# Optimization experiments

Measured on AMD Instinct MI355X. Metric: run time of the kernel, lower is better.

## Reference

```python
import jax, jax.numpy as jnp
import numpy as np

N = 50000


def gcn_conv(x, W, b, src, dst, deg_inv_sqrt):
    # h = x @ W, then symmetric-normalized aggregation with self-loops
    h = x @ W  # [N, out]
    norm = deg_inv_sqrt[src] * deg_inv_sqrt[dst]  # [E]
    agg = jax.ops.segment_sum(h[src] * norm[:, None], dst, num_segments=N)
    # self-loop contribution: norm_ii = deg_inv_sqrt[i]^2
    agg = agg + h * (deg_inv_sqrt * deg_inv_sqrt)[:, None]
    return agg + b


def setup_inputs() -> dict:
    key = jax.random.key(0)
    ks = jax.random.split(key, 8)
    F_in, H, C = 128, 128, 64
    x = jax.random.normal(ks[0], (N, F_in), dtype=jnp.float32)
    edge_index = jax.random.randint(ks[1], (2, 800000), 0, N, dtype=jnp.int64)
    s = 1.0 / np.sqrt(F_in)
    W1 = jax.random.uniform(ks[2], (F_in, H), jnp.float32, -s, s)
    b1 = jnp.zeros((H,), jnp.float32)
    W2 = jax.random.uniform(ks[3], (H, H), jnp.float32, -s, s)
    b2 = jnp.zeros((H,), jnp.float32)
    W3 = jax.random.uniform(ks[4], (H, C), jnp.float32, -s, s)
    b3 = jnp.zeros((C,), jnp.float32)
    return {"x": x, "edge_index": edge_index, "W1": W1, "b1": b1,
            "W2": W2, "b2": b2, "W3": W3, "b3": b3}


def reference(x, edge_index, W1, b1, W2, b2, W3, b3):
    src, dst = edge_index[0], edge_index[1]
    # degree with self-loops (edge weight 1): deg[i] = in-degree + 1
    deg = jnp.zeros((N,), x.dtype).at[dst].add(1.0) + 1.0
    dinv = jax.lax.rsqrt(deg)
    h = gcn_conv(x, W1, b1, src, dst, dinv)
    h = jax.nn.relu(h)  # dropout p=0 / eval -> identity
    h = gcn_conv(h, W2, b2, src, dst, dinv)
    h = jax.nn.relu(h)
    h = gcn_conv(h, W3, b3, src, dst, dinv)
    return jax.nn.log_softmax(h, axis=-1)
```

## Files before the change

kernel.cpp:

```cpp
#include <hip/hip_runtime.h>
#include <math.h>

typedef short short8 __attribute__((ext_vector_type(8)));
typedef float floatx4 __attribute__((ext_vector_type(4)));

__device__ __forceinline__ float4 ld4(const float* p) { return *reinterpret_cast<const float4*>(p); }
__device__ __forceinline__ void st4(float* p, float4 v) { *reinterpret_cast<float4*>(p) = v; }

__device__ __forceinline__ float bf2f(unsigned int u) { return __uint_as_float(u << 16); }
__device__ __forceinline__ unsigned int f2bf1(float f) {
    unsigned int x = __float_as_uint(f);
    return (x + 0x7fffu + ((x >> 16) & 1u)) >> 16;
}
__device__ __forceinline__ unsigned int f2bf2(float lo, float hi) {
    return f2bf1(lo) | (f2bf1(hi) << 16);
}
__device__ __forceinline__ void unpack8(uint4 v, float* f) {
    f[0] = bf2f(v.x & 0xffffu); f[1] = bf2f(v.x >> 16);
    f[2] = bf2f(v.y & 0xffffu); f[3] = bf2f(v.y >> 16);
    f[4] = bf2f(v.z & 0xffffu); f[5] = bf2f(v.z >> 16);
    f[6] = bf2f(v.w & 0xffffu); f[7] = bf2f(v.w >> 16);
}

__global__ __launch_bounds__(256) void k_count(const int* __restrict__ dst, int* __restrict__ deg,
                                               int* __restrict__ rank, int E) {
    int e = blockIdx.x * 256 + threadIdx.x;
    if (e < E) rank[e] = atomicAdd(&deg[dst[e]], 1);
}

__global__ __launch_bounds__(256) void k_reduce256(const int* __restrict__ deg, int* __restrict__ bsum, int n) {
    __shared__ int s[256];
    int t = threadIdx.x;
    int i = blockIdx.x * 256 + t;
    s[t] = (i < n) ? deg[i] : 0;
    __syncthreads();
    for (int off = 128; off > 0; off >>= 1) {
        if (t < off) s[t] += s[t + off];
        __syncthreads();
    }
    if (t == 0) bsum[blockIdx.x] = s[0];
}

__global__ __launch_bounds__(256) void k_scan_small(const int* __restrict__ bsum, int* __restrict__ boff, int nb) {
    __shared__ int s[256];
    int t = threadIdx.x;
    int v = (t < nb) ? bsum[t] : 0;
    s[t] = v;
    __syncthreads();
    for (int off = 1; off < 256; off <<= 1) {
        int x = (t >= off) ? s[t - off] : 0;
        __syncthreads();
        s[t] += x;
        __syncthreads();
    }
    if (t < nb) boff[t] = s[t] - v;
}

__global__ __launch_bounds__(256) void k_scan_final(const int* __restrict__ deg, const int* __restrict__ boff,
                                                    int* __restrict__ row_off, float* __restrict__ dinv, int n) {
    __shared__ int s[256];
    int t = threadIdx.x;
    int i = blockIdx.x * 256 + t;
    int v = (i < n) ? deg[i] : 0;
    s[t] = v;
    __syncthreads();
    for (int off = 1; off < 256; off <<= 1) {
        int x = (t >= off) ? s[t - off] : 0;
        __syncthreads();
        s[t] += x;
        __syncthreads();
    }
    int incl = s[t] + boff[blockIdx.x];
    if (i < n) {
        row_off[i] = incl - v;
        dinv[i]    = 1.0f / sqrtf((float)v + 1.0f);
        if (i == n - 1) row_off[n] = incl;
    }
}

__global__ __launch_bounds__(256) void k_fill(const int* __restrict__ src, const int* __restrict__ dst,
                                              const int* __restrict__ rank, const int* __restrict__ roff,
                                              const float* __restrict__ dinv, int2* __restrict__ cpair, int E) {
    int e = blockIdx.x * 256 + threadIdx.x;
    if (e < E) {
        int s = src[e], d = dst[e];
        int pos = roff[d] + rank[e];
        cpair[pos] = make_int2(s, __float_as_int(dinv[s] * dinv[d]));
    }
}

__global__ __launch_bounds__(256) void k_prepW(const float* __restrict__ W1, const float* __restrict__ W2,
                                               const float* __restrict__ W3, unsigned short* __restrict__ Wt1,
                                               unsigned short* __restrict__ Wt2, unsigned short* __restrict__ Wt3) {
    int t = blockIdx.x * 256 + threadIdx.x;
    if (t < 16384) {
        int k = t & 127, n = t >> 7;
        Wt1[n * 128 + k] = (unsigned short)f2bf1(W1[(size_t)k * 128 + n]);
    } else if (t < 32768) {
        int u = t - 16384;
        int k = u & 127, n = u >> 7;
        Wt2[n * 128 + k] = (unsigned short)f2bf1(W2[(size_t)k * 128 + n]);
    } else if (t < 40960) {
        int u = t - 32768;
        int k = u & 127, n = u >> 7;
        Wt3[n * 128 + k] = (unsigned short)f2bf1(W3[(size_t)k * 64 + n]);
    }
}

template <int NC, bool XF32>
__global__ __launch_bounds__(256) void k_gemm_mfma(const void* __restrict__ Xv, const unsigned short* __restrict__ Wt,
                                                   unsigned short* __restrict__ O, int nrows) {
    constexpr int LDR = 136;
    __shared__ unsigned short sX[64 * LDR];
    __shared__ unsigned short sB[NC * LDR];

    const int tid  = threadIdx.x;
    const int row0 = blockIdx.x * 64;

    if constexpr (XF32) {
        const float* X = (const float*)Xv;
#pragma unroll
        for (int i = 0; i < 4; ++i) {
            int idx = tid + i * 256;
            int r = idx >> 4, c8 = idx & 15;
            int grow = row0 + r;
            uint4 v = make_uint4(0, 0, 0, 0);
            if (grow < nrows) {
                float4 a = ld4(X + (size_t)grow * 128 + c8 * 8);
                float4 b = ld4(X + (size_t)grow * 128 + c8 * 8 + 4);
                v = make_uint4(f2bf2(a.x, a.y), f2bf2(a.z, a.w), f2bf2(b.x, b.y), f2bf2(b.z, b.w));
            }
            *reinterpret_cast<uint4*>(&sX[r * LDR + c8 * 8]) = v;
        }
    } else {
        const unsigned short* X = (const unsigned short*)Xv;
#pragma unroll
        for (int i = 0; i < 4; ++i) {
            int idx = tid + i * 256;
            int r = idx >> 4, c8 = idx & 15;
            int grow = row0 + r;
            uint4 v = make_uint4(0, 0, 0, 0);
            if (grow < nrows) v = *reinterpret_cast<const uint4*>(X + (size_t)grow * 128 + c8 * 8);
            *reinterpret_cast<uint4*>(&sX[r * LDR + c8 * 8]) = v;
        }
    }
#pragma unroll
    for (int i = 0; i < NC / 16; ++i) {
        int idx = tid + i * 256;
        int n = idx >> 4, c8 = idx & 15;
        *reinterpret_cast<uint4*>(&sB[n * LDR + c8 * 8]) =
            *reinterpret_cast<const uint4*>(Wt + (size_t)n * 128 + c8 * 8);
    }
    __syncthreads();

    const int lane = tid & 63;
    const int wave = tid >> 6;
    const int l15  = lane & 15;
    const int quad = lane >> 4;

    floatx4 acc[NC / 16];
#pragma unroll
    for (int j = 0; j < NC / 16; ++j) acc[j] = (floatx4){0.f, 0.f, 0.f, 0.f};

    const unsigned short* xbase = &sX[(wave * 16 + l15) * LDR + quad * 8];
#pragma unroll
    for (int kk = 0; kk < 4; ++kk) {
        short8 xb = *reinterpret_cast<const short8*>(xbase + kk * 32);
#pragma unroll
        for (int j = 0; j < NC / 16; ++j) {
            short8 wa = *reinterpret_cast<const short8*>(&sB[(j * 16 + l15) * LDR + quad * 8 + kk * 32]);
            acc[j] = __builtin_amdgcn_mfma_f32_16x16x32_bf16(wa, xb, acc[j], 0, 0, 0);
        }
    }

    int xrow = row0 + wave * 16 + l15;
    if (xrow < nrows) {
#pragma unroll
        for (int j = 0; j < NC / 16; ++j) {
            uint2 o = make_uint2(f2bf2(acc[j][0], acc[j][1]), f2bf2(acc[j][2], acc[j][3]));
            *reinterpret_cast<uint2*>(O + (size_t)xrow * NC + j * 16 + quad * 4) = o;
        }
    }
}

__global__ __launch_bounds__(256) void k_agg_relu(const unsigned short* __restrict__ H, const int* __restrict__ roff,
                                                  const int2* __restrict__ cpair, const float* __restrict__ dinv,
                                                  const float* __restrict__ bias, unsigned short* __restrict__ O, int n) {
    int t    = blockIdx.x * 256 + threadIdx.x;
    int node = t >> 4;
    int f8   = (t & 15) * 8;
    if (node >= n) return;

    float di = dinv[node];
    float sc = di * di;
    float a[8];
    {
        uint4 hv = *reinterpret_cast<const uint4*>(H + (size_t)node * 128 + f8);
        float h[8];
        unpack8(hv, h);
#pragma unroll
        for (int i = 0; i < 8; ++i) a[i] = h[i] * sc;
    }

    int e  = roff[node];
    int e1 = roff[node + 1];
    for (; e + 3 < e1; e += 4) {
        int2 p[4];
        uint4 v[4];
#pragma unroll
        for (int u = 0; u < 4; ++u) p[u] = cpair[e + u];
#pragma unroll
        for (int u = 0; u < 4; ++u) v[u] = *reinterpret_cast<const uint4*>(H + (size_t)p[u].x * 128 + f8);
#pragma unroll
        for (int u = 0; u < 4; ++u) {
            float nu = __int_as_float(p[u].y);
            float g[8];
            unpack8(v[u], g);
#pragma unroll
            for (int i = 0; i < 8; ++i) a[i] += g[i] * nu;
        }
    }
    for (; e < e1; ++e) {
        int2 p0 = cpair[e];
        float n0 = __int_as_float(p0.y);
        uint4 v0 = *reinterpret_cast<const uint4*>(H + (size_t)p0.x * 128 + f8);
        float g0[8];
        unpack8(v0, g0);
#pragma unroll
        for (int i = 0; i < 8; ++i) a[i] += g0[i] * n0;
    }

    float4 b0 = ld4(bias + f8);
    float4 b1 = ld4(bias + f8 + 4);
    float bb[8] = {b0.x, b0.y, b0.z, b0.w, b1.x, b1.y, b1.z, b1.w};
#pragma unroll
    for (int i = 0; i < 8; ++i) a[i] = fmaxf(a[i] + bb[i], 0.0f);

    uint4 ov = make_uint4(f2bf2(a[0], a[1]), f2bf2(a[2], a[3]), f2bf2(a[4], a[5]), f2bf2(a[6], a[7]));
    *reinterpret_cast<uint4*>(O + (size_t)node * 128 + f8) = ov;
}

__global__ __launch_bounds__(256) void k_agg_softmax(const unsigned short* __restrict__ H, const int* __restrict__ roff,
                                                     const int2* __restrict__ cpair, const float* __restrict__ dinv,
                                                     const float* __restrict__ bias, float* __restrict__ O, int n) {
    int t    = blockIdx.x * 256 + threadIdx.x;
    int node = t >> 3;
    int f8   = (t & 7) * 8;
    if (node >= n) return;

    float di = dinv[node];
    float sc = di * di;
    float a[8];
    {
        uint4 hv = *reinterpret_cast<const uint4*>(H + (size_t)node * 64 + f8);
        float h[8];
        unpack8(hv, h);
#pragma unroll
        for (int i = 0; i < 8; ++i) a[i] = h[i] * sc;
    }

    int e  = roff[node];
    int e1 = roff[node + 1];
    for (; e + 3 < e1; e += 4) {
        int2 p[4];
        uint4 v[4];
#pragma unroll
        for (int u = 0; u < 4; ++u) p[u] = cpair[e + u];
#pragma unroll
        for (int u = 0; u < 4; ++u) v[u] = *reinterpret_cast<const uint4*>(H + (size_t)p[u].x * 64 + f8);
#pragma unroll
        for (int u = 0; u < 4; ++u) {
            float nu = __int_as_float(p[u].y);
            float g[8];
            unpack8(v[u], g);
#pragma unroll
            for (int i = 0; i < 8; ++i) a[i] += g[i] * nu;
        }
    }
    for (; e < e1; ++e) {
        int2 p0 = cpair[e];
        float n0 = __int_as_float(p0.y);
        uint4 v0 = *reinterpret_cast<const uint4*>(H + (size_t)p0.x * 64 + f8);
        float g0[8];
        unpack8(v0, g0);
#pragma unroll
        for (int i = 0; i < 8; ++i) a[i] += g0[i] * n0;
    }

    float4 b0 = ld4(bias + f8);
    float4 b1 = ld4(bias + f8 + 4);
    float bb[8] = {b0.x, b0.y, b0.z, b0.w, b1.x, b1.y, b1.z, b1.w};
    float v[8];
#pragma unroll
    for (int i = 0; i < 8; ++i) v[i] = a[i] + bb[i];

    float m = v[0];
#pragma unroll
    for (int i = 1; i < 8; ++i) m = fmaxf(m, v[i]);
    m = fmaxf(m, __shfl_xor(m, 1));
    m = fmaxf(m, __shfl_xor(m, 2));
    m = fmaxf(m, __shfl_xor(m, 4));

    float ssum = 0.0f;
#pragma unroll
    for (int i = 0; i < 8; ++i) ssum += expf(v[i] - m);
    ssum += __shfl_xor(ssum, 1);
    ssum += __shfl_xor(ssum, 2);
    ssum += __shfl_xor(ssum, 4);
    float ls = logf(ssum);

    float* op = O + (size_t)node * 64 + f8;
    st4(op, make_float4(v[0] - m - ls, v[1] - m - ls, v[2] - m - ls, v[3] - m - ls));
    st4(op + 4, make_float4(v[4] - m - ls, v[5] - m - ls, v[6] - m - ls, v[7] - m - ls));
}

extern "C" void kernel_launch(void* const* d_in, const int* in_sizes, int n_in,
                              void* d_out, int out_size, void* d_ws, size_t ws_size,
                              hipStream_t stream) {
    const float* x  = (const float*)d_in[0];
    const int*   ei = (const int*)d_in[1];
    const float* W1 = (const float*)d_in[2];
    const float* b1 = (const float*)d_in[3];
    const float* W2 = (const float*)d_in[4];
    const float* b2 = (const float*)d_in[5];
    const float* W3 = (const float*)d_in[6];
    const float* b3 = (const float*)d_in[7];
    float* out = (float*)d_out;

    const int N = in_sizes[0] / 128;
    const int E = in_sizes[1] / 2;
    const int* src = ei;
    const int* dst = ei + E;

    char* ws = (char*)d_ws;
    size_t off = 0;
    auto alloc = [&](size_t bytes) -> char* {
        char* p = ws + off;
        off = (off + bytes + 255) & ~(size_t)255;
        return p;
    };
    int nb = (N + 255) / 256;
    int*   deg     = (int*)alloc((size_t)N * 4);
    int*   row_off = (int*)alloc(((size_t)N + 1) * 4);
    float* dinv    = (float*)alloc((size_t)N * 4);
    int*   bsum    = (int*)alloc((size_t)nb * 4);
    int*   boff    = (int*)alloc((size_t)nb * 4);
    int*   rank    = (int*)alloc((size_t)E * 4);
    int2*  cpair   = (int2*)alloc((size_t)E * 8);
    unsigned short* Wt1  = (unsigned short*)alloc(128 * 128 * 2);
    unsigned short* Wt2  = (unsigned short*)alloc(128 * 128 * 2);
    unsigned short* Wt3  = (unsigned short*)alloc(64 * 128 * 2);
    unsigned short* bufA = (unsigned short*)alloc((size_t)N * 128 * 2);
    unsigned short* bufB = (unsigned short*)alloc((size_t)N * 128 * 2);
    unsigned short* bufC = (unsigned short*)alloc((size_t)N * 64 * 2);
    (void)ws_size; (void)n_in; (void)out_size;

    hipMemsetAsync(deg, 0, (size_t)N * 4, stream);
    k_count<<<(E + 255) / 256, 256, 0, stream>>>(dst, deg, rank, E);
    k_reduce256<<<nb, 256, 0, stream>>>(deg, bsum, N);
    k_scan_small<<<1, 256, 0, stream>>>(bsum, boff, nb);
    k_scan_final<<<nb, 256, 0, stream>>>(deg, boff, row_off, dinv, N);
    k_fill<<<(E + 255) / 256, 256, 0, stream>>>(src, dst, rank, row_off, dinv, cpair, E);

    k_prepW<<<(40960 + 255) / 256, 256, 0, stream>>>(W1, W2, W3, Wt1, Wt2, Wt3);

    int gemm_blocks = (N + 63) / 64;
    k_gemm_mfma<128, true><<<gemm_blocks, 256, 0, stream>>>(x, Wt1, bufA, N);
    k_agg_relu<<<((size_t)N * 16 + 255) / 256, 256, 0, stream>>>(bufA, row_off, cpair, dinv, b1, bufB, N);
    k_gemm_mfma<128, false><<<gemm_blocks, 256, 0, stream>>>(bufB, Wt2, bufA, N);
    k_agg_relu<<<((size_t)N * 16 + 255) / 256, 256, 0, stream>>>(bufA, row_off, cpair, dinv, b2, bufB, N);
    k_gemm_mfma<64, false><<<gemm_blocks, 256, 0, stream>>>(bufB, Wt3, bufC, N);
    k_agg_softmax<<<((size_t)N * 8 + 255) / 256, 256, 0, stream>>>(bufC, row_off, cpair, dinv, b3, out, N);
}
```

Before: 257.7 us.

## Fuse aggregation+ReLU with the next layer's GEMM and unroll gathers by eight

```diff
diff --git a/kernel.cpp b/kernel.cpp
--- a/kernel.cpp
+++ b/kernel.cpp
@@ -107,45 +107,30 @@
     }
 }
 
-template <int NC, bool XF32>
-__global__ __launch_bounds__(256) void k_gemm_mfma(const void* __restrict__ Xv, const unsigned short* __restrict__ Wt,
-                                                   unsigned short* __restrict__ O, int nrows) {
+__global__ __launch_bounds__(256) void k_gemm1(const float* __restrict__ X, const unsigned short* __restrict__ Wt,
+                                               unsigned short* __restrict__ O, int nrows) {
     constexpr int LDR = 136;
     __shared__ unsigned short sX[64 * LDR];
-    __shared__ unsigned short sB[NC * LDR];
+    __shared__ unsigned short sB[128 * LDR];
 
     const int tid  = threadIdx.x;
     const int row0 = blockIdx.x * 64;
 
-    if constexpr (XF32) {
-        const float* X = (const float*)Xv;
-#pragma unroll
-        for (int i = 0; i < 4; ++i) {
-            int idx = tid + i * 256;
-            int r = idx >> 4, c8 = idx & 15;
-            int grow = row0 + r;
-            uint4 v = make_uint4(0, 0, 0, 0);
-            if (grow < nrows) {
-                float4 a = ld4(X + (size_t)grow * 128 + c8 * 8);
-                float4 b = ld4(X + (size_t)grow * 128 + c8 * 8 + 4);
-                v = make_uint4(f2bf2(a.x, a.y), f2bf2(a.z, a.w), f2bf2(b.x, b.y), f2bf2(b.z, b.w));
-            }
-            *reinterpret_cast<uint4*>(&sX[r * LDR + c8 * 8]) = v;
-        }
-    } else {
-        const unsigned short* X = (const unsigned short*)Xv;
-#pragma unroll
-        for (int i = 0; i < 4; ++i) {
-            int idx = tid + i * 256;
-            int r = idx >> 4, c8 = idx & 15;
-            int grow = row0 + r;
-            uint4 v = make_uint4(0, 0, 0, 0);
-            if (grow < nrows) v = *reinterpret_cast<const uint4*>(X + (size_t)grow * 128 + c8 * 8);
-            *reinterpret_cast<uint4*>(&sX[r * LDR + c8 * 8]) = v;
-        }
-    }
-#pragma unroll
-    for (int i = 0; i < NC / 16; ++i) {
+#pragma unroll
+    for (int i = 0; i < 4; ++i) {
+        int idx = tid + i * 256;
+        int r = idx >> 4, c8 = idx & 15;
+        int grow = row0 + r;
+        uint4 v = make_uint4(0, 0, 0, 0);
+        if (grow < nrows) {
+            float4 a = ld4(X + (size_t)grow * 128 + c8 * 8);
+            float4 b = ld4(X + (size_t)grow * 128 + c8 * 8 + 4);
+            v = make_uint4(f2bf2(a.x, a.y), f2bf2(a.z, a.w), f2bf2(b.x, b.y), f2bf2(b.z, b.w));
+        }
+        *reinterpret_cast<uint4*>(&sX[r * LDR + c8 * 8]) = v;
+    }
+#pragma unroll
+    for (int i = 0; i < 8; ++i) {
         int idx = tid + i * 256;
         int n = idx >> 4, c8 = idx & 15;
         *reinterpret_cast<uint4*>(&sB[n * LDR + c8 * 8]) =
@@ -158,16 +143,16 @@
     const int l15  = lane & 15;
     const int quad = lane >> 4;
 
-    floatx4 acc[NC / 16];
-#pragma unroll
-    for (int j = 0; j < NC / 16; ++j) acc[j] = (floatx4){0.f, 0.f, 0.f, 0.f};
+    floatx4 acc[8];
+#pragma unroll
+    for (int j = 0; j < 8; ++j) acc[j] = (floatx4){0.f, 0.f, 0.f, 0.f};
 
     const unsigned short* xbase = &sX[(wave * 16 + l15) * LDR + quad * 8];
 #pragma unroll
     for (int kk = 0; kk < 4; ++kk) {
         short8 xb = *reinterpret_cast<const short8*>(xbase + kk * 32);
 #pragma unroll
-        for (int j = 0; j < NC / 16; ++j) {
+        for (int j = 0; j < 8; ++j) {
             short8 wa = *reinterpret_cast<const short8*>(&sB[(j * 16 + l15) * LDR + quad * 8 + kk * 32]);
             acc[j] = __builtin_amdgcn_mfma_f32_16x16x32_bf16(wa, xb, acc[j], 0, 0, 0);
         }
@@ -175,69 +160,124 @@
 
     int xrow = row0 + wave * 16 + l15;
     if (xrow < nrows) {
+#pragma unroll
+        for (int j = 0; j < 8; ++j) {
+            uint2 o = make_uint2(f2bf2(acc[j][0], acc[j][1]), f2bf2(acc[j][2], acc[j][3]));
+            *reinterpret_cast<uint2*>(O + (size_t)xrow * 128 + j * 16 + quad * 4) = o;
+        }
+    }
+}
+
+template <int NC>
+__global__ __launch_bounds__(256) void k_agg_gemm(const unsigned short* __restrict__ H, const int* __restrict__ roff,
+                                                  const int2* __restrict__ cpair, const float* __restrict__ dinv,
+                                                  const float* __restrict__ bias, const unsigned short* __restrict__ Wt,
+                                                  unsigned short* __restrict__ O, int n) {
+    constexpr int LDR = 136;
+    __shared__ unsigned short sX[64 * LDR];
+
+    const int tid  = threadIdx.x;
+    const int row0 = blockIdx.x * 64;
+    const int g    = tid >> 4;
+    const int f8   = (tid & 15) * 8;
+
+    float4 b0 = ld4(bias + f8);
+    float4 b1 = ld4(bias + f8 + 4);
+    float bb[8] = {b0.x, b0.y, b0.z, b0.w, b1.x, b1.y, b1.z, b1.w};
+
+#pragma unroll
+    for (int p = 0; p < 4; ++p) {
+        int node = row0 + p * 16 + g;
+        float a[8] = {0.f, 0.f, 0.f, 0.f, 0.f, 0.f, 0.f, 0.f};
+        if (node < n) {
+            float di = dinv[node];
+            float sc = di * di;
+            uint4 hv = *reinterpret_cast<const uint4*>(H + (size_t)node * 128 + f8);
+            float h[8];
+            unpack8(hv, h);
+#pragma unroll
+            for (int i = 0; i < 8; ++i) a[i] = h[i] * sc;
+
+            int e  = roff[node];
+            int e1 = roff[node + 1];
+            for (; e + 7 < e1; e += 8) {
+                int2 pr[8];
+                uint4 v[8];
+#pragma unroll
+                for (int u = 0; u < 8; ++u) pr[u] = cpair[e + u];
+#pragma unroll
+                for (int u = 0; u < 8; ++u) v[u] = *reinterpret_cast<const uint4*>(H + (size_t)pr[u].x * 128 + f8);
+#pragma unroll
+                for (int u = 0; u < 8; ++u) {
+                    float nu = __int_as_float(pr[u].y);
+                    float gg[8];
+                    unpack8(v[u], gg);
+#pragma unroll
+                    for (int i = 0; i < 8; ++i) a[i] += gg[i] * nu;
+                }
+            }
+            if (e + 3 < e1) {
+                int2 pr[4];
+                uint4 v[4];
+#pragma unroll
+                for (int u = 0; u < 4; ++u) pr[u] = cpair[e + u];
+#pragma unroll
+                for (int u = 0; u < 4; ++u) v[u] = *reinterpret_cast<const uint4*>(H + (size_t)pr[u].x * 128 + f8);
+#pragma unroll
+                for (int u = 0; u < 4; ++u) {
+                    float nu = __int_as_float(pr[u].y);
+                    float gg[8];
+                    unpack8(v[u], gg);
+#pragma unroll
+                    for (int i = 0; i < 8; ++i) a[i] += gg[i] * nu;
+                }
+                e += 4;
+            }
+            for (; e < e1; ++e) {
+                int2 p0 = cpair[e];
+                float n0 = __int_as_float(p0.y);
+                uint4 v0 = *reinterpret_cast<const uint4*>(H + (size_t)p0.x * 128 + f8);
+                float g0[8];
+                unpack8(v0, g0);
+#pragma unroll
+                for (int i = 0; i < 8; ++i) a[i] += g0[i] * n0;
+            }
+#pragma unroll
+            for (int i = 0; i < 8; ++i) a[i] = fmaxf(a[i] + bb[i], 0.0f);
+        }
+        uint4 ov = make_uint4(f2bf2(a[0], a[1]), f2bf2(a[2], a[3]), f2bf2(a[4], a[5]), f2bf2(a[6], a[7]));
+        *reinterpret_cast<uint4*>(&sX[(p * 16 + g) * LDR + f8]) = ov;
+    }
+    __syncthreads();
+
+    const int lane = tid & 63;
+    const int wave = tid >> 6;
+    const int l15  = lane & 15;
+    const int quad = lane >> 4;
+
+    floatx4 acc[NC / 16];
+#pragma unroll
+    for (int j = 0; j < NC / 16; ++j) acc[j] = (floatx4){0.f, 0.f, 0.f, 0.f};
+
+    const unsigned short* xbase = &sX[(wave * 16 + l15) * LDR + quad * 8];
+#pragma unroll
+    for (int kk = 0; kk < 4; ++kk) {
+        short8 xb = *reinterpret_cast<const short8*>(xbase + kk * 32);
+#pragma unroll
+        for (int j = 0; j < NC / 16; ++j) {
+            short8 wa = *reinterpret_cast<const short8*>(Wt + (size_t)(j * 16 + l15) * 128 + quad * 8 + kk * 32);
+            acc[j] = __builtin_amdgcn_mfma_f32_16x16x32_bf16(wa, xb, acc[j], 0, 0, 0);
+        }
+    }
+
+    int xrow = row0 + wave * 16 + l15;
+    if (xrow < n) {
 #pragma unroll
         for (int j = 0; j < NC / 16; ++j) {
             uint2 o = make_uint2(f2bf2(acc[j][0], acc[j][1]), f2bf2(acc[j][2], acc[j][3]));
             *reinterpret_cast<uint2*>(O + (size_t)xrow * NC + j * 16 + quad * 4) = o;
         }
     }
-}
-
-__global__ __launch_bounds__(256) void k_agg_relu(const unsigned short* __restrict__ H, const int* __restrict__ roff,
-                                                  const int2* __restrict__ cpair, const float* __restrict__ dinv,
-                                                  const float* __restrict__ bias, unsigned short* __restrict__ O, int n) {
-    int t    = blockIdx.x * 256 + threadIdx.x;
-    int node = t >> 4;
-    int f8   = (t & 15) * 8;
-    if (node >= n) return;
-
-    float di = dinv[node];
-    float sc = di * di;
-    float a[8];
-    {
-        uint4 hv = *reinterpret_cast<const uint4*>(H + (size_t)node * 128 + f8);
-        float h[8];
-        unpack8(hv, h);
-#pragma unroll
-        for (int i = 0; i < 8; ++i) a[i] = h[i] * sc;
-    }
-
-    int e  = roff[node];
-    int e1 = roff[node + 1];
-    for (; e + 3 < e1; e += 4) {
-        int2 p[4];
-        uint4 v[4];
-#pragma unroll
-        for (int u = 0; u < 4; ++u) p[u] = cpair[e + u];
-#pragma unroll
-        for (int u = 0; u < 4; ++u) v[u] = *reinterpret_cast<const uint4*>(H + (size_t)p[u].x * 128 + f8);
-#pragma unroll
-        for (int u = 0; u < 4; ++u) {
-            float nu = __int_as_float(p[u].y);
-            float g[8];
-            unpack8(v[u], g);
-#pragma unroll
-            for (int i = 0; i < 8; ++i) a[i] += g[i] * nu;
-        }
-    }
-    for (; e < e1; ++e) {
-        int2 p0 = cpair[e];
-        float n0 = __int_as_float(p0.y);
-        uint4 v0 = *reinterpret_cast<const uint4*>(H + (size_t)p0.x * 128 + f8);
-        float g0[8];
-        unpack8(v0, g0);
-#pragma unroll
-        for (int i = 0; i < 8; ++i) a[i] += g0[i] * n0;
-    }
-
-    float4 b0 = ld4(bias + f8);
-    float4 b1 = ld4(bias + f8 + 4);
-    float bb[8] = {b0.x, b0.y, b0.z, b0.w, b1.x, b1.y, b1.z, b1.w};
-#pragma unroll
-    for (int i = 0; i < 8; ++i) a[i] = fmaxf(a[i] + bb[i], 0.0f);
-
-    uint4 ov = make_uint4(f2bf2(a[0], a[1]), f2bf2(a[2], a[3]), f2bf2(a[4], a[5]), f2bf2(a[6], a[7]));
-    *reinterpret_cast<uint4*>(O + (size_t)node * 128 + f8) = ov;
 }
 
 __global__ __launch_bounds__(256) void k_agg_softmax(const unsigned short* __restrict__ H, const int* __restrict__ roff,
@@ -261,21 +301,38 @@
 
     int e  = roff[node];
     int e1 = roff[node + 1];
-    for (; e + 3 < e1; e += 4) {
-        int2 p[4];
+    for (; e + 7 < e1; e += 8) {
+        int2 pr[8];
+        uint4 v[8];
+#pragma unroll
+        for (int u = 0; u < 8; ++u) pr[u] = cpair[e + u];
+#pragma unroll
+        for (int u = 0; u < 8; ++u) v[u] = *reinterpret_cast<const uint4*>(H + (size_t)pr[u].x * 64 + f8);
+#pragma unroll
+        for (int u = 0; u < 8; ++u) {
+            float nu = __int_as_float(pr[u].y);
+            float gg[8];
+            unpack8(v[u], gg);
+#pragma unroll
+            for (int i = 0; i < 8; ++i) a[i] += gg[i] * nu;
+        }
+    }
+    if (e + 3 < e1) {
+        int2 pr[4];
         uint4 v[4];
 #pragma unroll
-        for (int u = 0; u < 4; ++u) p[u] = cpair[e + u];
-#pragma unroll
-        for (int u = 0; u < 4; ++u) v[u] = *reinterpret_cast<const uint4*>(H + (size_t)p[u].x * 64 + f8);
+        for (int u = 0; u < 4; ++u) pr[u] = cpair[e + u];
+#pragma unroll
+        for (int u = 0; u < 4; ++u) v[u] = *reinterpret_cast<const uint4*>(H + (size_t)pr[u].x * 64 + f8);
 #pragma unroll
         for (int u = 0; u < 4; ++u) {
-            float nu = __int_as_float(p[u].y);
-            float g[8];
-            unpack8(v[u], g);
-#pragma unroll
-            for (int i = 0; i < 8; ++i) a[i] += g[i] * nu;
-        }
+            float nu = __int_as_float(pr[u].y);
+            float gg[8];
+            unpack8(v[u], gg);
+#pragma unroll
+            for (int i = 0; i < 8; ++i) a[i] += gg[i] * nu;
+        }
+        e += 4;
     }
     for (; e < e1; ++e) {
         int2 p0 = cpair[e];
@@ -364,11 +421,9 @@
 
     k_prepW<<<(40960 + 255) / 256, 256, 0, stream>>>(W1, W2, W3, Wt1, Wt2, Wt3);
 
-    int gemm_blocks = (N + 63) / 64;
-    k_gemm_mfma<128, true><<<gemm_blocks, 256, 0, stream>>>(x, Wt1, bufA, N);
-    k_agg_relu<<<((size_t)N * 16 + 255) / 256, 256, 0, stream>>>(bufA, row_off, cpair, dinv, b1, bufB, N);
-    k_gemm_mfma<128, false><<<gemm_blocks, 256, 0, stream>>>(bufB, Wt2, bufA, N);
-    k_agg_relu<<<((size_t)N * 16 + 255) / 256, 256, 0, stream>>>(bufA, row_off, cpair, dinv, b2, bufB, N);
-    k_gemm_mfma<64, false><<<gemm_blocks, 256, 0, stream>>>(bufB, Wt3, bufC, N);
+    int blocks64 = (N + 63) / 64;
+    k_gemm1<<<blocks64, 256, 0, stream>>>(x, Wt1, bufA, N);
+    k_agg_gemm<128><<<blocks64, 256, 0, stream>>>(bufA, row_off, cpair, dinv, b1, Wt2, bufB, N);
+    k_agg_gemm<64><<<blocks64, 256, 0, stream>>>(bufB, row_off, cpair, dinv, b2, Wt3, bufC, N);
     k_agg_softmax<<<((size_t)N * 8 + 255) / 256, 256, 0, stream>>>(bufC, row_off, cpair, dinv, b3, out, N);
 }
```

Result: slower. 276.2 us (+7.2%).
